# Kernel optimization log

Measured on AMD Instinct MI355X. Metric: run time of the kernel, lower is better.

## Reference

```python
import jax, jax.numpy as jnp
import numpy as np

N_NODES = 50000
N_EDGES = 800000
IN_DIM = 256
OUT_DIM = 64
HEADS = 4
NEG_SLOPE = 0.2  # PyG GATConv default


def setup_inputs() -> dict:
    key = jax.random.key(0)
    k_x, k_e, k_w, k_as, k_ad = jax.random.split(key, 5)
    x = jax.random.normal(k_x, (N_NODES, IN_DIM), dtype=jnp.float32)
    edge_index = jax.random.randint(k_e, (2, N_EDGES), 0, N_NODES, dtype=jnp.int64)
    # Glorot-ish scaled params (as in PyG GATConv)
    W = jax.random.normal(k_w, (IN_DIM, HEADS * OUT_DIM), dtype=jnp.float32) / np.sqrt(IN_DIM)
    att_src = jax.random.normal(k_as, (HEADS, OUT_DIM), dtype=jnp.float32) / np.sqrt(OUT_DIM)
    att_dst = jax.random.normal(k_ad, (HEADS, OUT_DIM), dtype=jnp.float32) / np.sqrt(OUT_DIM)
    bias = jnp.zeros((HEADS * OUT_DIM,), dtype=jnp.float32)
    return {"x": x, "edge_index": edge_index, "W": W,
            "att_src": att_src, "att_dst": att_dst, "bias": bias}


def reference(x, edge_index, W, att_src, att_dst, bias):
    N = x.shape[0]
    H, C = att_src.shape
    # add self-loops (PyG GATConv default add_self_loops=True)
    loop = jnp.arange(N, dtype=edge_index.dtype)
    src = jnp.concatenate([edge_index[0], loop])  # [E+N] message sources j
    dst = jnp.concatenate([edge_index[1], loop])  # [E+N] message targets i

    xh = (x @ W).reshape(N, H, C)                 # [N, H, C]
    a_src = jnp.einsum('nhc,hc->nh', xh, att_src)  # [N, H]
    a_dst = jnp.einsum('nhc,hc->nh', xh, att_dst)  # [N, H]

    logits = jax.nn.leaky_relu(a_src[src] + a_dst[dst], NEG_SLOPE)  # [E+N, H]
    # segment softmax over incoming edges of each destination node
    seg_max = jax.ops.segment_max(logits, dst, num_segments=N)      # [N, H]
    e = jnp.exp(logits - seg_max[dst])
    seg_sum = jax.ops.segment_sum(e, dst, num_segments=N)           # [N, H]
    alpha = e / seg_sum[dst]                                        # [E+N, H]

    # weighted scatter-aggregate of source features
    msgs = alpha[:, :, None] * xh[src]                              # [E+N, H, C]
    out = jax.ops.segment_sum(msgs, dst, num_segments=N)            # [N, H, C]
    out = out.reshape(N, H * C) + bias                              # concat heads + bias
    # h.dim() == 2 here, so the original's mean(dim=1) branch is not taken
    return out
```

## Files before the change

### kernel.cpp

```cpp
#include <hip/hip_runtime.h>

#define NEG_SLOPE 0.2f
#define LRELU(x) ((x) > 0.0f ? (x) : NEG_SLOPE * (x))

typedef short short8 __attribute__((ext_vector_type(8)));
typedef float f32x4v __attribute__((ext_vector_type(4)));

__device__ __forceinline__ unsigned short f2bf(float f) {
  unsigned int u = __float_as_uint(f);
  unsigned int r = (u + 0x7FFFu + ((u >> 16) & 1u)) >> 16;
  return (unsigned short)r;
}

__device__ __forceinline__ float bf2f(unsigned short u) {
  return __uint_as_float(((unsigned int)u) << 16);
}

__device__ __forceinline__ void gload_lds16(const void* g, void* l) {
  __builtin_amdgcn_global_load_lds(
      (const __attribute__((address_space(1))) unsigned int*)g,
      (__attribute__((address_space(3))) unsigned int*)l, 16, 0, 0);
}

#define CBX 1536
#define CBC 512
#define CBW 64
#define CBF 512

__global__ __launch_bounds__(256) void fused_pre(
    const float* __restrict__ X, unsigned short* __restrict__ Xb,
    const float* __restrict__ W, unsigned short* __restrict__ Wtb,
    const int* __restrict__ ei, int* __restrict__ deg,
    int totalX, int validX, int E) {
  int b = blockIdx.x;
  int tid = threadIdx.x;
  if (b < CBX) {
    for (int i = (b * 256 + tid) * 4; i < totalX; i += CBX * 256 * 4) {
      ushort4 o;
      if (i < validX) {
        float4 v = *reinterpret_cast<const float4*>(X + i);
        o.x = f2bf(v.x); o.y = f2bf(v.y); o.z = f2bf(v.z); o.w = f2bf(v.w);
      } else {
        o.x = o.y = o.z = o.w = 0;
      }
      *reinterpret_cast<ushort4*>(Xb + i) = o;
    }
  } else if (b < CBX + CBC) {
    int bb = b - CBX;
    for (int e = bb * 256 + tid; e < E; e += CBC * 256)
      atomicAdd(&deg[ei[E + e]], 1);
  } else {
    int bb = b - CBX - CBC;
    for (int idx = bb * 256 + tid; idx < 256 * 256; idx += CBW * 256) {
      int n = idx >> 8, k = idx & 255;
      Wtb[n * 256 + k] = f2bf(W[k * 256 + n]);
    }
  }
}

__global__ __launch_bounds__(1024) void scan1_kernel(const int* __restrict__ deg,
                                                     int* __restrict__ row_start,
                                                     int* __restrict__ bsum, int N) {
  __shared__ int buf[1024];
  int i = blockIdx.x * 1024 + (int)threadIdx.x;
  int v = (i < N) ? deg[i] : 0;
  buf[threadIdx.x] = v;
  __syncthreads();
  int run = v;
  for (int off = 1; off < 1024; off <<= 1) {
    int t = ((int)threadIdx.x >= off) ? buf[threadIdx.x - off] : 0;
    __syncthreads();
    run += t;
    buf[threadIdx.x] = run;
    __syncthreads();
  }
  if (i < N) row_start[i] = run - v;
  if (threadIdx.x == 1023) bsum[blockIdx.x] = run;
}

__global__ __launch_bounds__(1024) void scan_off(int* __restrict__ row_start,
                                                 const int* __restrict__ bsum,
                                                 int nb, int N) {
  __shared__ int s_off;
  int b = blockIdx.x;
  if (threadIdx.x < 64) {
    int acc = 0;
    for (int j = (int)threadIdx.x; j < b; j += 64) acc += bsum[j];
    for (int off = 32; off; off >>= 1) acc += __shfl_down(acc, off, 64);
    if (threadIdx.x == 0) s_off = acc;
  }
  __syncthreads();
  int off = s_off;
  int i = b * 1024 + (int)threadIdx.x;
  if (i < N) row_start[i] += off;
  if (b == nb - 1 && threadIdx.x == 0) row_start[N] = off + bsum[b];
}

__global__ __launch_bounds__(256) void fused_main(
    const unsigned short* __restrict__ Xb, const unsigned short* __restrict__ Wtb,
    const float* __restrict__ attS, const float* __restrict__ attD,
    unsigned short* __restrict__ XHb, float* __restrict__ a_src,
    float* __restrict__ a_dst,
    const int* __restrict__ ei, const int* __restrict__ row_start,
    int* __restrict__ cursor, int* __restrict__ csr_src,
    int nGemm, int E, int N) {
  __shared__ unsigned short lA[128 * 32];
  __shared__ unsigned short lB[128 * 32];
  const int bid = blockIdx.x;
  const int tid = threadIdx.x;

  if (bid >= nGemm) {
    int bb = bid - nGemm;
    for (int e = bb * 256 + tid; e < E; e += CBF * 256) {
      int d = ei[E + e];
      int slot = row_start[d] + atomicAdd(&cursor[d], 1);
      csr_src[slot] = ei[e];
    }
    return;
  }

  const int lane = tid & 63;
  const int wave = tid >> 6;
  const int n0 = (bid & 1) * 128;
  const int m0 = (bid >> 1) * 128;
  const int wr = (wave >> 1) * 64;
  const int wc = (wave & 1) * 64;

  f32x4v acc[4][4];
#pragma unroll
  for (int i = 0; i < 4; ++i)
#pragma unroll
    for (int j = 0; j < 4; ++j) acc[i][j] = (f32x4v)(0.0f);

  const int srow = tid >> 2;
  const int skb = (tid & 3) * 16;
  const char* XbC = (const char*)Xb;
  const char* WtC = (const char*)Wtb;
  char* lAc = (char*)&lA[0];
  char* lBc = (char*)&lB[0];
  const int ldsB0 = wave * 1024;
  const int lr = lane & 15;
  const int hq = lane >> 4;
  const int kq = hq * 16;

  for (int k0 = 0; k0 < 256; k0 += 32) {
    const size_t kbyte = (size_t)k0 * 2 + skb;
    gload_lds16(XbC + (size_t)(m0 + srow) * 512 + kbyte, lAc + ldsB0);
    gload_lds16(XbC + (size_t)(m0 + srow + 64) * 512 + kbyte, lAc + ldsB0 + 4096);
    gload_lds16(WtC + (size_t)(n0 + srow) * 512 + kbyte, lBc + ldsB0);
    gload_lds16(WtC + (size_t)(n0 + srow + 64) * 512 + kbyte, lBc + ldsB0 + 4096);
    __syncthreads();

    short8 a[4], b[4];
#pragma unroll
    for (int i = 0; i < 4; ++i)
      a[i] = *reinterpret_cast<const short8*>(lAc + (wr + i * 16 + lr) * 64 + kq);
#pragma unroll
    for (int j = 0; j < 4; ++j)
      b[j] = *reinterpret_cast<const short8*>(lBc + (wc + j * 16 + lr) * 64 + kq);
#pragma unroll
    for (int i = 0; i < 4; ++i)
#pragma unroll
      for (int j = 0; j < 4; ++j)
        acc[i][j] = __builtin_amdgcn_mfma_f32_16x16x32_bf16(a[i], b[j], acc[i][j], 0, 0, 0);
    __syncthreads();
  }

  const int h = (n0 + wc) >> 6;
  float ws_[4], wd_[4];
#pragma unroll
  for (int j = 0; j < 4; ++j) {
    ws_[j] = attS[h * 64 + j * 16 + lr];
    wd_[j] = attD[h * 64 + j * 16 + lr];
  }
  const int rbase = m0 + wr + hq * 4;

#pragma unroll
  for (int i = 0; i < 4; ++i) {
#pragma unroll
    for (int r = 0; r < 4; ++r) {
      float ps = 0.f, pd = 0.f;
#pragma unroll
      for (int j = 0; j < 4; ++j) {
        ps += acc[i][j][r] * ws_[j];
        pd += acc[i][j][r] * wd_[j];
      }
#pragma unroll
      for (int off = 1; off < 16; off <<= 1) {
        ps += __shfl_xor(ps, off, 64);
        pd += __shfl_xor(pd, off, 64);
      }
      int row = rbase + i * 16 + r;
      if (lr == 0 && row < N) {
        a_src[row * 4 + h] = ps;
        a_dst[row * 4 + h] = pd;
      }
    }
  }

#pragma unroll
  for (int i = 0; i < 4; ++i)
#pragma unroll
    for (int j = 0; j < 4; ++j) {
      int col = n0 + wc + j * 16 + lr;
#pragma unroll
      for (int r = 0; r < 4; ++r)
        XHb[(size_t)(rbase + i * 16 + r) * 256 + col] = f2bf(acc[i][j][r]);
    }
}

__global__ __launch_bounds__(256) void gat_agg(
    const unsigned short* __restrict__ XHb, const float* __restrict__ a_src,
    const float* __restrict__ a_dst, const int* __restrict__ row_start,
    const int* __restrict__ csr_src, const float* __restrict__ bias,
    float* __restrict__ out, int N) {
  int wid = threadIdx.x >> 6;
  int lane = threadIdx.x & 63;
  int node = blockIdx.x * 4 + wid;
  if (node >= N) return;

  int h = lane >> 4;
  int c = lane << 2;
  const unsigned short* __restrict__ xrow = XHb + c;
  float ad_h = a_dst[node * 4 + h];
  float as_h = a_src[node * 4 + h];
  float wself = __expf(LRELU(as_h + ad_h));

  int start = row_start[node];
  int end = row_start[node + 1];

  ushort4 sv = *reinterpret_cast<const ushort4*>(xrow + (size_t)node * 256);
  float4 acc;
  acc.x = wself * bf2f(sv.x); acc.y = wself * bf2f(sv.y);
  acc.z = wself * bf2f(sv.z); acc.w = wself * bf2f(sv.w);
  float sw = wself;

  int p = start;
  for (; p + 4 <= end; p += 4) {
    int s0 = csr_src[p];
    int s1 = csr_src[p + 1];
    int s2 = csr_src[p + 2];
    int s3 = csr_src[p + 3];
    float a0 = a_src[s0 * 4 + h] + ad_h;
    float a1 = a_src[s1 * 4 + h] + ad_h;
    float a2 = a_src[s2 * 4 + h] + ad_h;
    float a3 = a_src[s3 * 4 + h] + ad_h;
    ushort4 u0 = *reinterpret_cast<const ushort4*>(xrow + (size_t)s0 * 256);
    ushort4 u1 = *reinterpret_cast<const ushort4*>(xrow + (size_t)s1 * 256);
    ushort4 u2 = *reinterpret_cast<const ushort4*>(xrow + (size_t)s2 * 256);
    ushort4 u3 = *reinterpret_cast<const ushort4*>(xrow + (size_t)s3 * 256);
    float w0 = __expf(LRELU(a0));
    float w1 = __expf(LRELU(a1));
    float w2 = __expf(LRELU(a2));
    float w3 = __expf(LRELU(a3));
    acc.x += w0 * bf2f(u0.x); acc.y += w0 * bf2f(u0.y);
    acc.z += w0 * bf2f(u0.z); acc.w += w0 * bf2f(u0.w);
    acc.x += w1 * bf2f(u1.x); acc.y += w1 * bf2f(u1.y);
    acc.z += w1 * bf2f(u1.z); acc.w += w1 * bf2f(u1.w);
    acc.x += w2 * bf2f(u2.x); acc.y += w2 * bf2f(u2.y);
    acc.z += w2 * bf2f(u2.z); acc.w += w2 * bf2f(u2.w);
    acc.x += w3 * bf2f(u3.x); acc.y += w3 * bf2f(u3.y);
    acc.z += w3 * bf2f(u3.z); acc.w += w3 * bf2f(u3.w);
    sw += (w0 + w1) + (w2 + w3);
  }
  for (; p < end; ++p) {
    int s0 = csr_src[p];
    float a0 = a_src[s0 * 4 + h] + ad_h;
    ushort4 u0 = *reinterpret_cast<const ushort4*>(xrow + (size_t)s0 * 256);
    float w0 = __expf(LRELU(a0));
    acc.x += w0 * bf2f(u0.x); acc.y += w0 * bf2f(u0.y);
    acc.z += w0 * bf2f(u0.z); acc.w += w0 * bf2f(u0.w);
    sw += w0;
  }

  float inv = 1.0f / sw;
  float4 b = reinterpret_cast<const float4*>(bias)[lane];
  float4 o;
  o.x = acc.x * inv + b.x; o.y = acc.y * inv + b.y;
  o.z = acc.z * inv + b.z; o.w = acc.w * inv + b.w;
  *reinterpret_cast<float4*>(out + (size_t)node * 256 + c) = o;
}

extern "C" void kernel_launch(void* const* d_in, const int* in_sizes, int n_in,
                              void* d_out, int out_size, void* d_ws, size_t ws_size,
                              hipStream_t stream) {
  const float* x    = (const float*)d_in[0];
  const int*   ei   = (const int*)d_in[1];
  const float* Wm   = (const float*)d_in[2];
  const float* attS = (const float*)d_in[3];
  const float* attD = (const float*)d_in[4];
  const float* bias = (const float*)d_in[5];
  float* out = (float*)d_out;

  const int N = in_sizes[0] / 256;
  const int E = in_sizes[1] / 2;
  const int Mp = (N + 127) / 128 * 128;
  const int nb = (N + 1023) / 1024;

  char* w = (char*)d_ws;
  unsigned short* XHb = (unsigned short*)w;  w += (size_t)Mp * 256 * 2;
  unsigned short* Xb  = (unsigned short*)w;  w += (size_t)Mp * 256 * 2;
  unsigned short* Wtb = (unsigned short*)w;  w += (size_t)256 * 256 * 2;
  float* a_src = (float*)w;                  w += (size_t)N * 4 * 4;
  float* a_dst = (float*)w;                  w += (size_t)N * 4 * 4;
  int* deg = (int*)w;                        w += (size_t)N * 4;
  int* cursor = (int*)w;                     w += (size_t)N * 4;
  int* row_start = (int*)w;                  w += ((size_t)(N + 1) * 4 + 255) / 256 * 256;
  int* bsum = (int*)w;                       w += ((size_t)nb * 4 + 255) / 256 * 256;
  int* csr_src = (int*)w;                    w += (size_t)E * 4;

  hipMemsetAsync(deg, 0, (size_t)2 * N * 4, stream);

  fused_pre<<<CBX + CBC + CBW, 256, 0, stream>>>(x, Xb, Wm, Wtb, ei, deg,
                                                 Mp * 256, N * 256, E);

  scan1_kernel<<<nb, 1024, 0, stream>>>(deg, row_start, bsum, N);
  scan_off<<<nb, 1024, 0, stream>>>(row_start, bsum, nb, N);

  const int nGemm = 2 * (Mp / 128);
  fused_main<<<nGemm + CBF, 256, 0, stream>>>(Xb, Wtb, attS, attD, XHb, a_src, a_dst,
                                              ei, row_start, cursor, csr_src,
                                              nGemm, E, N);

  gat_agg<<<(N + 3) / 4, 256, 0, stream>>>(XHb, a_src, a_dst, row_start, csr_src,
                                           bias, out, N);
}
```

Before: 175.3 us.

## Split each wavefront into two half-waves processing alternate edges with 16-byte loads

The aggregation kernel now has each 32-lane half of a wavefront cover a full 256-column bf16 row with 8 elements per lane, using 16-byte loads. The two halves take interleaved edges, so each loop iteration covers 8 edges instead of 4, and the partial sums are combined with a cross-half shuffle at the end. This doubles memory-level parallelism per wave and widens the gather loads, which should better hide the latency of the random row gathers. In exchange it adds shuffle reductions and more accumulator registers, and the remainder loop is now a predicated fixed 4-step unroll.

```diff
diff --git a/kernel.cpp b/kernel.cpp
--- a/kernel.cpp
+++ b/kernel.cpp
@@ -4,6 +4,7 @@
 #define LRELU(x) ((x) > 0.0f ? (x) : NEG_SLOPE * (x))
 
 typedef short short8 __attribute__((ext_vector_type(8)));
+typedef unsigned short ushort8 __attribute__((ext_vector_type(8)));
 typedef float f32x4v __attribute__((ext_vector_type(4)));
 
 __device__ __forceinline__ unsigned short f2bf(float f) {
@@ -219,66 +220,88 @@
   int node = blockIdx.x * 4 + wid;
   if (node >= N) return;
 
-  int h = lane >> 4;
-  int c = lane << 2;
+  const int half = lane >> 5;
+  const int l5 = lane & 31;
+  const int h = l5 >> 3;
+  const int c = l5 << 3;
   const unsigned short* __restrict__ xrow = XHb + c;
+
   float ad_h = a_dst[node * 4 + h];
   float as_h = a_src[node * 4 + h];
-  float wself = __expf(LRELU(as_h + ad_h));
 
   int start = row_start[node];
   int end = row_start[node + 1];
 
-  ushort4 sv = *reinterpret_cast<const ushort4*>(xrow + (size_t)node * 256);
-  float4 acc;
-  acc.x = wself * bf2f(sv.x); acc.y = wself * bf2f(sv.y);
-  acc.z = wself * bf2f(sv.z); acc.w = wself * bf2f(sv.w);
-  float sw = wself;
+  float acc[8];
+  float sw = 0.f;
+  if (half == 0) {
+    float wself = __expf(LRELU(as_h + ad_h));
+    ushort8 sv = *reinterpret_cast<const ushort8*>(xrow + (size_t)node * 256);
+#pragma unroll
+    for (int k = 0; k < 8; ++k) acc[k] = wself * bf2f(sv[k]);
+    sw = wself;
+  } else {
+#pragma unroll
+    for (int k = 0; k < 8; ++k) acc[k] = 0.f;
+  }
 
   int p = start;
-  for (; p + 4 <= end; p += 4) {
-    int s0 = csr_src[p];
-    int s1 = csr_src[p + 1];
-    int s2 = csr_src[p + 2];
-    int s3 = csr_src[p + 3];
+  for (; p + 8 <= end; p += 8) {
+    int s0 = csr_src[p + half];
+    int s1 = csr_src[p + 2 + half];
+    int s2 = csr_src[p + 4 + half];
+    int s3 = csr_src[p + 6 + half];
     float a0 = a_src[s0 * 4 + h] + ad_h;
     float a1 = a_src[s1 * 4 + h] + ad_h;
     float a2 = a_src[s2 * 4 + h] + ad_h;
     float a3 = a_src[s3 * 4 + h] + ad_h;
-    ushort4 u0 = *reinterpret_cast<const ushort4*>(xrow + (size_t)s0 * 256);
-    ushort4 u1 = *reinterpret_cast<const ushort4*>(xrow + (size_t)s1 * 256);
-    ushort4 u2 = *reinterpret_cast<const ushort4*>(xrow + (size_t)s2 * 256);
-    ushort4 u3 = *reinterpret_cast<const ushort4*>(xrow + (size_t)s3 * 256);
+    ushort8 u0 = *reinterpret_cast<const ushort8*>(xrow + (size_t)s0 * 256);
+    ushort8 u1 = *reinterpret_cast<const ushort8*>(xrow + (size_t)s1 * 256);
+    ushort8 u2 = *reinterpret_cast<const ushort8*>(xrow + (size_t)s2 * 256);
+    ushort8 u3 = *reinterpret_cast<const ushort8*>(xrow + (size_t)s3 * 256);
     float w0 = __expf(LRELU(a0));
     float w1 = __expf(LRELU(a1));
     float w2 = __expf(LRELU(a2));
     float w3 = __expf(LRELU(a3));
-    acc.x += w0 * bf2f(u0.x); acc.y += w0 * bf2f(u0.y);
-    acc.z += w0 * bf2f(u0.z); acc.w += w0 * bf2f(u0.w);
-    acc.x += w1 * bf2f(u1.x); acc.y += w1 * bf2f(u1.y);
-    acc.z += w1 * bf2f(u1.z); acc.w += w1 * bf2f(u1.w);
-    acc.x += w2 * bf2f(u2.x); acc.y += w2 * bf2f(u2.y);
-    acc.z += w2 * bf2f(u2.z); acc.w += w2 * bf2f(u2.w);
-    acc.x += w3 * bf2f(u3.x); acc.y += w3 * bf2f(u3.y);
-    acc.z += w3 * bf2f(u3.z); acc.w += w3 * bf2f(u3.w);
+#pragma unroll
+    for (int k = 0; k < 8; ++k) {
+      acc[k] += w0 * bf2f(u0[k]);
+      acc[k] += w1 * bf2f(u1[k]);
+      acc[k] += w2 * bf2f(u2[k]);
+      acc[k] += w3 * bf2f(u3[k]);
+    }
     sw += (w0 + w1) + (w2 + w3);
   }
-  for (; p < end; ++p) {
-    int s0 = csr_src[p];
-    float a0 = a_src[s0 * 4 + h] + ad_h;
-    ushort4 u0 = *reinterpret_cast<const ushort4*>(xrow + (size_t)s0 * 256);
-    float w0 = __expf(LRELU(a0));
-    acc.x += w0 * bf2f(u0.x); acc.y += w0 * bf2f(u0.y);
-    acc.z += w0 * bf2f(u0.z); acc.w += w0 * bf2f(u0.w);
-    sw += w0;
-  }
-
-  float inv = 1.0f / sw;
-  float4 b = reinterpret_cast<const float4*>(bias)[lane];
-  float4 o;
-  o.x = acc.x * inv + b.x; o.y = acc.y * inv + b.y;
-  o.z = acc.z * inv + b.z; o.w = acc.w * inv + b.w;
-  *reinterpret_cast<float4*>(out + (size_t)node * 256 + c) = o;
+#pragma unroll
+  for (int k = 0; k < 4; ++k) {
+    int idx = p + 2 * k + half;
+    if (idx < end) {
+      int s = csr_src[idx];
+      float aa = a_src[s * 4 + h] + ad_h;
+      ushort8 u = *reinterpret_cast<const ushort8*>(xrow + (size_t)s * 256);
+      float ww = __expf(LRELU(aa));
+#pragma unroll
+      for (int q = 0; q < 8; ++q) acc[q] += ww * bf2f(u[q]);
+      sw += ww;
+    }
+  }
+
+  sw += __shfl_xor(sw, 32, 64);
+#pragma unroll
+  for (int k = 0; k < 8; ++k) acc[k] += __shfl_xor(acc[k], 32, 64);
+
+  if (half == 0) {
+    float inv = 1.0f / sw;
+    float4 b0 = *reinterpret_cast<const float4*>(bias + c);
+    float4 b1 = *reinterpret_cast<const float4*>(bias + c + 4);
+    float4 o0, o1;
+    o0.x = acc[0] * inv + b0.x; o0.y = acc[1] * inv + b0.y;
+    o0.z = acc[2] * inv + b0.z; o0.w = acc[3] * inv + b0.w;
+    o1.x = acc[4] * inv + b1.x; o1.y = acc[5] * inv + b1.y;
+    o1.z = acc[6] * inv + b1.z; o1.w = acc[7] * inv + b1.w;
+    *reinterpret_cast<float4*>(out + (size_t)node * 256 + c) = o0;
+    *reinterpret_cast<float4*>(out + (size_t)node * 256 + c + 4) = o1;
+  }
 }
 
 extern "C" void kernel_launch(void* const* d_in, const int* in_sizes, int n_in,
```

New measurement: 173.3 us. No clear change (-1.1%).
